# Optimization experiments

Measured on AMD Instinct MI355X. Metric: run time of the kernel, lower is better.

## Reference

```python
import jax, jax.numpy as jnp
import numpy as np

EMBED = 1024
HEADS = 16
HEAD_DIM = EMBED // HEADS


def setup_inputs() -> dict:
    key = jax.random.key(0)
    ks = jax.random.split(key, 11)
    B, S, D = 2, 2048, EMBED
    scale = 1.0 / np.sqrt(D)
    inp = {
        "q": jax.random.normal(ks[0], (B, S, D), jnp.float32),
        "k": jax.random.normal(ks[1], (B, S, D), jnp.float32),
        "v": jax.random.normal(ks[2], (B, S, D), jnp.float32),
        "Wq": jax.random.normal(ks[3], (D, D), jnp.float32) * scale,
        "bq": jnp.zeros((D,), jnp.float32),
        "Wk": jax.random.normal(ks[4], (D, D), jnp.float32) * scale,
        "bk": jnp.zeros((D,), jnp.float32),
        "Wv": jax.random.normal(ks[5], (D, D), jnp.float32) * scale,
        "bv": jnp.zeros((D,), jnp.float32),
        "Wo": jax.random.normal(ks[6], (D, D), jnp.float32) * scale,
        "bo": jnp.zeros((D,), jnp.float32),
    }
    return inp


def _split_heads(x):
    b, n, c = x.shape
    return x.reshape(b, n, HEADS, c // HEADS).transpose(0, 2, 1, 3)  # [b,h,n,dh]


def reference(q, k, v, Wq, bq, Wk, bk, Wv, bv, Wo, bo):
    qh = _split_heads(q @ Wq + bq)
    kh = _split_heads(k @ Wk + bk)
    vh = _split_heads(v @ Wv + bv)
    scale = 1.0 / jnp.sqrt(jnp.asarray(HEAD_DIM, qh.dtype))
    att = jnp.einsum("bhqd,bhkd->bhqk", qh, kh) * scale
    att = jax.nn.softmax(att, axis=-1)
    out = jnp.einsum("bhqk,bhkd->bhqd", att, vh)
    b, h, n, dh = out.shape
    out = out.transpose(0, 2, 1, 3).reshape(b, n, h * dh)
    return out @ Wo + bo
```

## Files before the change

kernel.cpp:

```cpp
#include <hip/hip_runtime.h>
#include <hip/hip_bf16.h>
#include <stdint.h>

typedef unsigned short u16;
typedef __bf16 bf16x8 __attribute__((ext_vector_type(8)));
typedef float f32x4 __attribute__((ext_vector_type(4)));
typedef float f32x16 __attribute__((ext_vector_type(16)));
typedef unsigned int u32x4 __attribute__((ext_vector_type(4)));
typedef unsigned int u32x2 __attribute__((ext_vector_type(2)));

#define S_LEN 2048
#define DMODEL 1024
#define NHEAD 16
#define DHEAD 64
#define MROWS 4096
#define EXP2SCALE 0.180336880112f

__device__ __forceinline__ u16 f2b(float f) {
  __hip_bfloat16 h = __float2bfloat16(f);
  union { __hip_bfloat16 h; u16 u; } c;
  c.h = h;
  return c.u;
}
__device__ __forceinline__ unsigned int pk2(float lo, float hi) {
  return (unsigned int)f2b(lo) | ((unsigned int)f2b(hi) << 16);
}
__device__ __forceinline__ unsigned int cvtpk(float a, float b) {
  unsigned int r;
  asm("v_cvt_pk_bf16_f32 %0, %1, %2" : "=v"(r) : "v"(a), "v"(b));
  return r;
}
__device__ __forceinline__ void plswap(unsigned int &a, unsigned int &b) {
  auto r = __builtin_amdgcn_permlane32_swap((int)a, (int)b, false, false);
  a = (unsigned int)r[0];
  b = (unsigned int)r[1];
}

__device__ __forceinline__ void gload16(const void* g, void* l) {
  __builtin_amdgcn_global_load_lds(
      (const __attribute__((address_space(1))) unsigned int*)(uintptr_t)g,
      (__attribute__((address_space(3))) unsigned int*)(uintptr_t)l,
      16, 0, 0);
}

__global__ __launch_bounds__(256) void prep(
    const float* __restrict__ q, const float* __restrict__ k, const float* __restrict__ v,
    const float* __restrict__ Wq, const float* __restrict__ Wk,
    const float* __restrict__ Wv, const float* __restrict__ Wo,
    u16* __restrict__ Qx, u16* __restrict__ Kx, u16* __restrict__ Vx,
    u16* __restrict__ Wqt, u16* __restrict__ Wkt,
    u16* __restrict__ Wvt, u16* __restrict__ Wot) {
  __shared__ u16 tile[64][65];
  const int z = blockIdx.z;
  const int tid = threadIdx.x;
  if (z < 3) {
    const float* src = (z == 0) ? q : (z == 1) ? k : v;
    u16* dst = (z == 0) ? Qx : (z == 1) ? Kx : Vx;
    const size_t i8 = ((size_t)blockIdx.x * 256 + tid) * 8;
    float4 a = *(const float4*)(src + i8);
    float4 b = *(const float4*)(src + i8 + 4);
    u16 o[8];
    o[0] = f2b(a.x); o[1] = f2b(a.y); o[2] = f2b(a.z); o[3] = f2b(a.w);
    o[4] = f2b(b.x); o[5] = f2b(b.y); o[6] = f2b(b.z); o[7] = f2b(b.w);
    *(u32x4*)(dst + i8) = *(const u32x4*)o;
    return;
  }
  if (blockIdx.x >= 256) return;
  const int zz = z - 3;
  const float* W = (zz == 0) ? Wq : (zz == 1) ? Wk : (zz == 2) ? Wv : Wo;
  u16* Wt = (zz == 0) ? Wqt : (zz == 1) ? Wkt : (zz == 2) ? Wvt : Wot;
  const int n0 = (blockIdx.x & 15) * 64, k0 = (blockIdx.x >> 4) * 64;
#pragma unroll
  for (int j = 0; j < 16; j++) {
    int idx = j * 256 + tid;
    int r = idx >> 6, c = idx & 63;
    tile[r][c] = f2b(W[(size_t)(k0 + r) * DMODEL + n0 + c]);
  }
  __syncthreads();
#pragma unroll
  for (int j = 0; j < 16; j++) {
    int idx = j * 256 + tid;
    int r = idx >> 6, c = idx & 63;
    Wt[(size_t)(n0 + r) * DMODEL + k0 + c] = tile[c][r];
  }
}

template <int MODE>
__device__ __forceinline__ void gemm_body(const u16* __restrict__ A,
                                          const u16* __restrict__ Bt,
                                          const float* __restrict__ bias,
                                          void* __restrict__ Cv) {
  constexpr int K = DMODEL;
  __shared__ u16 As[128 * 32];
  __shared__ u16 Bs[128 * 32];
  const int tid = threadIdx.x;
  const int wave = tid >> 6, lane = tid & 63;
  const int quad = lane >> 4, l15 = lane & 15;
  const int wr = wave >> 1, wc = wave & 1;
  const int lid = blockIdx.y * 8 + blockIdx.x;
  const int sw = (lid & 7) * 32 + (lid >> 3);
  const int bcol = sw & 7, brow = sw >> 3;

  f32x4 acc[4][4] = {};

  for (int k0 = 0; k0 < K; k0 += 32) {
    __syncthreads();
#pragma unroll
    for (int t = 0; t < 2; t++) {
      const int slot = t * 256 + wave * 64 + lane;
      const int row = slot >> 2;
      const int col = (slot & 3) << 3;
      const int ldsb = (t * 256 + wave * 64) * 8;
      gload16(A + (size_t)(brow * 128 + row) * K + k0 + col, As + ldsb);
      gload16(Bt + (size_t)(bcol * 128 + row) * K + k0 + col, Bs + ldsb);
    }
    __syncthreads();

    bf16x8 af[4], bfm[4];
#pragma unroll
    for (int i = 0; i < 4; i++)
      af[i] = *(const bf16x8*)(As + (wr * 64 + i * 16 + l15) * 32 + quad * 8);
#pragma unroll
    for (int j = 0; j < 4; j++)
      bfm[j] = *(const bf16x8*)(Bs + (wc * 64 + j * 16 + l15) * 32 + quad * 8);
#pragma unroll
    for (int i = 0; i < 4; i++)
#pragma unroll
      for (int j = 0; j < 4; j++)
        acc[i][j] = __builtin_amdgcn_mfma_f32_16x16x32_bf16(af[i], bfm[j], acc[i][j], 0, 0, 0);
  }

#pragma unroll
  for (int i = 0; i < 4; i++)
#pragma unroll
    for (int j = 0; j < 4; j++) {
      const int col = bcol * 128 + wc * 64 + j * 16 + l15;
      const float bv = bias[col];
      if (MODE == 2) {
        const int srow = brow * 128 + wr * 64 + i * 16 + quad * 4;
        const int bb = srow >> 11, s = srow & (S_LEN - 1);
        u32x2 pd;
        pd.x = pk2(acc[i][j][0] + bv, acc[i][j][1] + bv);
        pd.y = pk2(acc[i][j][2] + bv, acc[i][j][3] + bv);
        *(u32x2*)((u16*)Cv + ((size_t)(bb * 1024 + col)) * S_LEN + s) = pd;
      } else {
#pragma unroll
        for (int r = 0; r < 4; r++) {
          const int row = brow * 128 + wr * 64 + i * 16 + quad * 4 + r;
          if (MODE == 1)
            ((float*)Cv)[(size_t)row * DMODEL + col] = acc[i][j][r] + bv;
          else if (MODE == 3)
            ((u16*)Cv)[(size_t)row * DMODEL + col] = f2b((acc[i][j][r] + bv) * EXP2SCALE);
          else
            ((u16*)Cv)[(size_t)row * DMODEL + col] = f2b(acc[i][j][r] + bv);
        }
      }
    }
}

__global__ __launch_bounds__(256) void gemm_qkv(
    const u16* __restrict__ Qx, const u16* __restrict__ Kx, const u16* __restrict__ Vx,
    const u16* __restrict__ Wqt, const u16* __restrict__ Wkt, const u16* __restrict__ Wvt,
    const float* __restrict__ bq, const float* __restrict__ bk, const float* __restrict__ bv,
    u16* __restrict__ Qp, u16* __restrict__ Kp, u16* __restrict__ Vt) {
  const int z = blockIdx.z;
  if (z == 2) {
    gemm_body<2>(Vx, Wvt, bv, Vt);
  } else if (z == 0) {
    gemm_body<3>(Qx, Wqt, bq, Qp);
  } else {
    gemm_body<0>(Kx, Wkt, bk, Kp);
  }
}

__global__ __launch_bounds__(256) void gemm_out(
    const u16* __restrict__ A, const u16* __restrict__ Bt,
    const float* __restrict__ bias, float* __restrict__ C) {
  gemm_body<1>(A, Bt, bias, C);
}

#define ISSUE_KV(ksb, vsb)              \
  do {                                  \
    gload16(pK0, (ksb) + dstu);         \
    gload16(pK1, (ksb) + 2048 + dstu);  \
    gload16(pV0, (vsb) + dstu);         \
    gload16(pV1, (vsb) + 2048 + dstu);  \
    pK0 += 64 * DMODEL; pK1 += 64 * DMODEL; \
    pV0 += 64; pV1 += 64;               \
  } while (0)

#define TILE_COMPUTE(ksb, vsb)                                                     \
  do {                                                                             \
    f32x16 sA = {}, sB = {};                                                       \
    __builtin_amdgcn_s_setprio(1);                                                 \
    _Pragma("unroll") for (int c = 0; c < 4; c++) {                                \
      bf16x8 ka0 = *(const bf16x8*)((ksb) + off[c]);                               \
      bf16x8 ka1 = *(const bf16x8*)((ksb) + off[c] + 2048);                        \
      sA = __builtin_amdgcn_mfma_f32_32x32x16_bf16(ka0, qf[c], sA, 0, 0, 0);       \
      sB = __builtin_amdgcn_mfma_f32_32x32x16_bf16(ka1, qf[c], sB, 0, 0, 0);       \
    }                                                                              \
    __builtin_amdgcn_s_setprio(0);                                                 \
    bf16x8 pf[4];                                                                  \
    _Pragma("unroll") for (int kb = 0; kb < 2; kb++) {                             \
      const f32x16 s = kb ? sB : sA;                                               \
      unsigned int cc[8];                                                          \
      _Pragma("unroll") for (int m = 0; m < 8; m++)                                \
        cc[m] = cvtpk(__builtin_amdgcn_exp2f(s[2 * m]),                            \
                      __builtin_amdgcn_exp2f(s[2 * m + 1]));                       \
      plswap(cc[0], cc[2]);                                                        \
      plswap(cc[1], cc[3]);                                                        \
      plswap(cc[4], cc[6]);                                                        \
      plswap(cc[5], cc[7]);                                                        \
      union { unsigned int u[4]; bf16x8 v; } f0, f1;                               \
      f0.u[0] = cc[0]; f0.u[1] = cc[1]; f0.u[2] = cc[2]; f0.u[3] = cc[3];          \
      f1.u[0] = cc[4]; f1.u[1] = cc[5]; f1.u[2] = cc[6]; f1.u[3] = cc[7];          \
      pf[2 * kb] = f0.v; pf[2 * kb + 1] = f1.v;                                    \
    }                                                                              \
    __builtin_amdgcn_s_setprio(1);                                                 \
    _Pragma("unroll") for (int g = 0; g < 4; g++) {                                \
      bf16x8 v0 = *(const bf16x8*)((vsb) + off[g]);                                \
      bf16x8 v1 = *(const bf16x8*)((vsb) + off[g] + 2048);                         \
      lacc  = __builtin_amdgcn_mfma_f32_32x32x16_bf16(pf[g], ones, lacc, 0, 0, 0); \
      oacc0 = __builtin_amdgcn_mfma_f32_32x32x16_bf16(pf[g], v0, oacc0, 0, 0, 0);  \
      oacc1 = __builtin_amdgcn_mfma_f32_32x32x16_bf16(pf[g], v1, oacc1, 0, 0, 0);  \
    }                                                                              \
    __builtin_amdgcn_s_setprio(0);                                                 \
  } while (0)

__global__ __launch_bounds__(256) void attn(const u16* __restrict__ Qp,
                                            const u16* __restrict__ Kp,
                                            const u16* __restrict__ Vt,
                                            u16* __restrict__ Op) {
  __shared__ u16 Ks0[64 * 64], Ks1[64 * 64];
  __shared__ u16 Vs0[64 * 64], Vs1[64 * 64];

  const int tid = threadIdx.x;
  const int wave = tid >> 6, lane = tid & 63;
  const int row31 = lane & 31, hl = lane >> 5;

  const int id = blockIdx.x + (blockIdx.y << 4) + (blockIdx.z << 8);
  const int sw = ((id & 7) << 6) + (id >> 3);
  const int qt = sw & 15, h = (sw >> 4) & 15, b = sw >> 8;
  const int s0 = qt * 128;

  const size_t baseK = ((size_t)(b * S_LEN)) * DMODEL + h * DHEAD;
  const size_t baseV = ((size_t)((b * NHEAD + h) * DHEAD)) * S_LEN;

  const int r0 = tid >> 3;
  const int cg = (tid & 7) ^ (r0 & 7);
  const u16* pK0 = Kp + baseK + (size_t)r0 * DMODEL + cg * 8;
  const u16* pK1 = pK0 + (size_t)32 * DMODEL;
  const u16* pV0 = Vt + baseV + (size_t)r0 * S_LEN + cg * 8;
  const u16* pV1 = pV0 + (size_t)32 * S_LEN;
  const int dstu = wave * 512;

  int off[4];
#pragma unroll
  for (int c = 0; c < 4; c++)
    off[c] = row31 * 64 + ((((c << 1) + hl) ^ (row31 & 7)) << 3);

  bf16x8 ones;
  {
    union { u16 a[8]; bf16x8 v; } c;
#pragma unroll
    for (int j = 0; j < 8; j++) c.a[j] = 0x3F80;
    ones = c.v;
  }

  bf16x8 qf[4];
#pragma unroll
  for (int c = 0; c < 4; c++)
    qf[c] = *(const bf16x8*)(Qp +
        ((size_t)(b * S_LEN + s0 + wave * 32 + row31)) * DMODEL +
        h * DHEAD + c * 16 + hl * 8);

  f32x16 oacc0 = {}, oacc1 = {};
  f32x16 lacc = {};

  ISSUE_KV(Ks0, Vs0);

#pragma unroll 1
  for (int kt = 0; kt < 32; kt += 2) {
    __syncthreads();
    ISSUE_KV(Ks1, Vs1);
    TILE_COMPUTE(Ks0, Vs0);
    __syncthreads();
    if (kt + 2 < 32) ISSUE_KV(Ks0, Vs0);
    TILE_COMPUTE(Ks1, Vs1);
  }

#pragma unroll
  for (int r = 0; r < 16; r++) {
    const float inv = 1.0f / lacc[r];
    const int qrow = (r & 3) + 8 * (r >> 2) + 4 * hl;
    const size_t rb = ((size_t)(b * S_LEN + s0 + wave * 32 + qrow)) * DMODEL + h * DHEAD;
    Op[rb + row31]      = f2b(oacc0[r] * inv);
    Op[rb + 32 + row31] = f2b(oacc1[r] * inv);
  }
}

extern "C" void kernel_launch(void* const* d_in, const int* in_sizes, int n_in,
                              void* d_out, int out_size, void* d_ws, size_t ws_size,
                              hipStream_t stream) {
  const float* q  = (const float*)d_in[0];
  const float* k  = (const float*)d_in[1];
  const float* v  = (const float*)d_in[2];
  const float* Wq = (const float*)d_in[3];
  const float* bq = (const float*)d_in[4];
  const float* Wk = (const float*)d_in[5];
  const float* bk = (const float*)d_in[6];
  const float* Wv = (const float*)d_in[7];
  const float* bv = (const float*)d_in[8];
  const float* Wo = (const float*)d_in[9];
  const float* bo = (const float*)d_in[10];

  char* w = (char*)d_ws;
  const size_t WSZ = (size_t)DMODEL * DMODEL * 2;
  const size_t XSZ = (size_t)MROWS * DMODEL * 2;
  u16* Wqt = (u16*)(w);
  u16* Wkt = (u16*)(w + WSZ);
  u16* Wvt = (u16*)(w + 2 * WSZ);
  u16* Wot = (u16*)(w + 3 * WSZ);
  u16* Qx  = (u16*)(w + 4 * WSZ);
  u16* Kx  = (u16*)(w + 4 * WSZ + XSZ);
  u16* Vx  = (u16*)(w + 4 * WSZ + 2 * XSZ);
  u16* Qp  = (u16*)(w + 4 * WSZ + 3 * XSZ);
  u16* Kp  = (u16*)(w + 4 * WSZ + 4 * XSZ);
  u16* Vt  = (u16*)(w + 4 * WSZ + 5 * XSZ);
  u16* Op  = (u16*)(w + 4 * WSZ + 6 * XSZ);

  prep<<<dim3(2048, 1, 7), 256, 0, stream>>>(q, k, v, Wq, Wk, Wv, Wo,
                                             Qx, Kx, Vx, Wqt, Wkt, Wvt, Wot);
  gemm_qkv<<<dim3(8, 32, 3), 256, 0, stream>>>(Qx, Kx, Vx, Wqt, Wkt, Wvt,
                                               bq, bk, bv, Qp, Kp, Vt);
  attn<<<dim3(16, 16, 2), 256, 0, stream>>>(Qp, Kp, Vt, Op);
  gemm_out<<<dim3(8, 32, 1), 256, 0, stream>>>(Op, Wot, bo, (float*)d_out);
}
```

Measured before the change: 221.7 us.

## Split attention KV range across wave pairs and read V directly from global

The attention kernel now uses 64-query tiles with two wave groups that each process half of the key sequence, merging partial outputs and row sums through shared memory at the end. The grid doubles to 1024 blocks to improve occupancy and CU coverage. V is no longer staged in LDS; each wave loads its V fragments straight from global memory, which removes the V LDS traffic but relies on cache hits for the repeated reads. The design also adds a final reduction step and skips max-subtraction, the same as before.

After: 254.5 us. 14.8% more time.

```diff
diff --git a/kernel.cpp b/kernel.cpp
--- a/kernel.cpp
+++ b/kernel.cpp
@@ -179,17 +179,7 @@
   gemm_body<1>(A, Bt, bias, C);
 }
 
-#define ISSUE_KV(ksb, vsb)              \
-  do {                                  \
-    gload16(pK0, (ksb) + dstu);         \
-    gload16(pK1, (ksb) + 2048 + dstu);  \
-    gload16(pV0, (vsb) + dstu);         \
-    gload16(pV1, (vsb) + 2048 + dstu);  \
-    pK0 += 64 * DMODEL; pK1 += 64 * DMODEL; \
-    pV0 += 64; pV1 += 64;               \
-  } while (0)
-
-#define TILE_COMPUTE(ksb, vsb)                                                     \
+#define TILE_COMPUTE(ksb, kt)                                                      \
   do {                                                                             \
     f32x16 sA = {}, sB = {};                                                       \
     __builtin_amdgcn_s_setprio(1);                                                 \
@@ -218,8 +208,8 @@
     }                                                                              \
     __builtin_amdgcn_s_setprio(1);                                                 \
     _Pragma("unroll") for (int g = 0; g < 4; g++) {                                \
-      bf16x8 v0 = *(const bf16x8*)((vsb) + off[g]);                                \
-      bf16x8 v1 = *(const bf16x8*)((vsb) + off[g] + 2048);                         \
+      bf16x8 v0 = *(const bf16x8*)(pV + (size_t)(kt) * 64 + g * 16);               \
+      bf16x8 v1 = *(const bf16x8*)(pV + (size_t)32 * S_LEN + (kt) * 64 + g * 16);  \
       lacc  = __builtin_amdgcn_mfma_f32_32x32x16_bf16(pf[g], ones, lacc, 0, 0, 0); \
       oacc0 = __builtin_amdgcn_mfma_f32_32x32x16_bf16(pf[g], v0, oacc0, 0, 0, 0);  \
       oacc1 = __builtin_amdgcn_mfma_f32_32x32x16_bf16(pf[g], v1, oacc1, 0, 0, 0);  \
@@ -227,32 +217,37 @@
     __builtin_amdgcn_s_setprio(0);                                                 \
   } while (0)
 
+#define ISSUE_K(dst, ktg)                                                       \
+  do {                                                                          \
+    const u16* gp = pK + (size_t)(ktg) * 64 * DMODEL;                           \
+    _Pragma("unroll") for (int c = 0; c < 4; c++)                               \
+      gload16(gp + (size_t)c * 8 * DMODEL, (dst) + (qg * 32 + c * 8) * 64);     \
+  } while (0)
+
 __global__ __launch_bounds__(256) void attn(const u16* __restrict__ Qp,
                                             const u16* __restrict__ Kp,
                                             const u16* __restrict__ Vt,
                                             u16* __restrict__ Op) {
-  __shared__ u16 Ks0[64 * 64], Ks1[64 * 64];
-  __shared__ u16 Vs0[64 * 64], Vs1[64 * 64];
+  __shared__ u16 Ks[2][2][64 * 64];
 
   const int tid = threadIdx.x;
   const int wave = tid >> 6, lane = tid & 63;
   const int row31 = lane & 31, hl = lane >> 5;
-
-  const int id = blockIdx.x + (blockIdx.y << 4) + (blockIdx.z << 8);
-  const int sw = ((id & 7) << 6) + (id >> 3);
-  const int qt = sw & 15, h = (sw >> 4) & 15, b = sw >> 8;
-  const int s0 = qt * 128;
+  const int qg = wave & 1, kh = wave >> 1;
+
+  const int id = blockIdx.x + (blockIdx.y << 5) + (blockIdx.z << 9);
+  const int sw = ((id & 7) << 7) + (id >> 3);
+  const int qt = sw & 31, h = (sw >> 5) & 15, b = sw >> 9;
+  const int s0 = qt * 64;
 
   const size_t baseK = ((size_t)(b * S_LEN)) * DMODEL + h * DHEAD;
   const size_t baseV = ((size_t)((b * NHEAD + h) * DHEAD)) * S_LEN;
 
-  const int r0 = tid >> 3;
-  const int cg = (tid & 7) ^ (r0 & 7);
-  const u16* pK0 = Kp + baseK + (size_t)r0 * DMODEL + cg * 8;
-  const u16* pK1 = pK0 + (size_t)32 * DMODEL;
-  const u16* pV0 = Vt + baseV + (size_t)r0 * S_LEN + cg * 8;
-  const u16* pV1 = pV0 + (size_t)32 * S_LEN;
-  const int dstu = wave * 512;
+  const u16* pK = Kp + baseK +
+      (size_t)(kh * 1024 + qg * 32 + (lane >> 3)) * DMODEL +
+      (((lane & 7) ^ (lane >> 3)) << 3);
+
+  const u16* pV = Vt + baseV + (size_t)row31 * S_LEN + kh * 1024 + hl * 8;
 
   int off[4];
 #pragma unroll
@@ -271,31 +266,47 @@
 #pragma unroll
   for (int c = 0; c < 4; c++)
     qf[c] = *(const bf16x8*)(Qp +
-        ((size_t)(b * S_LEN + s0 + wave * 32 + row31)) * DMODEL +
+        ((size_t)(b * S_LEN + s0 + qg * 32 + row31)) * DMODEL +
         h * DHEAD + c * 16 + hl * 8);
 
   f32x16 oacc0 = {}, oacc1 = {};
   f32x16 lacc = {};
 
-  ISSUE_KV(Ks0, Vs0);
+  ISSUE_K(&Ks[kh][0][0], 0);
 
 #pragma unroll 1
-  for (int kt = 0; kt < 32; kt += 2) {
+  for (int kt = 0; kt < 16; kt += 2) {
     __syncthreads();
-    ISSUE_KV(Ks1, Vs1);
-    TILE_COMPUTE(Ks0, Vs0);
+    ISSUE_K(&Ks[kh][1][0], kt + 1);
+    TILE_COMPUTE(&Ks[kh][0][0], kt);
     __syncthreads();
-    if (kt + 2 < 32) ISSUE_KV(Ks0, Vs0);
-    TILE_COMPUTE(Ks1, Vs1);
-  }
-
-#pragma unroll
-  for (int r = 0; r < 16; r++) {
-    const float inv = 1.0f / lacc[r];
-    const int qrow = (r & 3) + 8 * (r >> 2) + 4 * hl;
-    const size_t rb = ((size_t)(b * S_LEN + s0 + wave * 32 + qrow)) * DMODEL + h * DHEAD;
-    Op[rb + row31]      = f2b(oacc0[r] * inv);
-    Op[rb + 32 + row31] = f2b(oacc1[r] * inv);
+    if (kt + 2 < 16) ISSUE_K(&Ks[kh][0][0], kt + 2);
+    TILE_COMPUTE(&Ks[kh][1][0], kt + 1);
+  }
+
+  __syncthreads();
+  float* M = ((float*)&Ks[0][0][0]) + qg * 3072;
+  if (kh == 1) {
+#pragma unroll
+    for (int r = 0; r < 16; r++) {
+      M[r * 64 + lane]        = oacc0[r];
+      M[1024 + r * 64 + lane] = oacc1[r];
+      M[2048 + r * 64 + lane] = lacc[r];
+    }
+  }
+  __syncthreads();
+  if (kh == 0) {
+#pragma unroll
+    for (int r = 0; r < 16; r++) {
+      const float o0 = oacc0[r] + M[r * 64 + lane];
+      const float o1 = oacc1[r] + M[1024 + r * 64 + lane];
+      const float ls = lacc[r] + M[2048 + r * 64 + lane];
+      const float inv = 1.0f / ls;
+      const int qrow = (r & 3) + 8 * (r >> 2) + 4 * hl;
+      const size_t rb = ((size_t)(b * S_LEN + s0 + qg * 32 + qrow)) * DMODEL + h * DHEAD;
+      Op[rb + row31]      = f2b(o0 * inv);
+      Op[rb + 32 + row31] = f2b(o1 * inv);
+    }
   }
 }
 
@@ -333,6 +344,6 @@
                                              Qx, Kx, Vx, Wqt, Wkt, Wvt, Wot);
   gemm_qkv<<<dim3(8, 32, 3), 256, 0, stream>>>(Qx, Kx, Vx, Wqt, Wkt, Wvt,
                                                bq, bk, bv, Qp, Kp, Vt);
-  attn<<<dim3(16, 16, 2), 256, 0, stream>>>(Qp, Kp, Vt, Op);
+  attn<<<dim3(32, 16, 2), 256, 0, stream>>>(Qp, Kp, Vt, Op);
   gemm_out<<<dim3(8, 32, 1), 256, 0, stream>>>(Op, Wot, bo, (float*)d_out);
 }
```
